# Optimization experiments

Measured on AMD Instinct MI355X. Metric: run time of the kernel, lower is better.

The kernel has to match this reference:

```python
import jax, jax.numpy as jnp
import numpy as np

N = 50000      # nodes
E = 800000     # edges (before self loops)
B = 64         # graphs in batch
D_IN, D_HID, D_LAT, N_CLS = 3, 128, 64, 2


def _gat_params(key, d_in, d_out, scale=0.1):
    k1, k2, k3 = jax.random.split(key, 3)
    return (jax.random.normal(k1, (d_in, d_out), jnp.float32) * scale,
            jax.random.normal(k2, (d_out,), jnp.float32) * scale,
            jax.random.normal(k3, (d_out,), jnp.float32) * scale,
            jnp.zeros((d_out,), jnp.float32))


def setup_inputs() -> dict:
    key = jax.random.key(0)
    ks = jax.random.split(key, 10)
    x = jax.random.normal(ks[0], (N, D_IN), jnp.float32)
    edge_index = jax.random.randint(ks[1], (2, E), 0, N, dtype=jnp.int64)
    batch = jnp.sort(jax.random.randint(ks[2], (N,), 0, B, dtype=jnp.int64))
    W1, a1s, a1d, b1 = _gat_params(ks[3], D_IN, D_HID)
    W2, a2s, a2d, b2 = _gat_params(ks[4], D_HID, D_LAT)
    W3, a3s, a3d, b3 = _gat_params(ks[5], D_LAT, D_HID)
    W4, a4s, a4d, b4 = _gat_params(ks[6], D_HID, D_IN)
    kc1, kc2 = jax.random.split(ks[7])
    Wc1 = jax.random.normal(kc1, (D_LAT, D_LAT // 2), jnp.float32) * 0.1
    bc1 = jnp.zeros((D_LAT // 2,), jnp.float32)
    Wc2 = jax.random.normal(kc2, (D_LAT // 2, N_CLS), jnp.float32) * 0.1
    bc2 = jnp.zeros((N_CLS,), jnp.float32)
    return dict(x=x, edge_index=edge_index, batch=batch,
                W1=W1, a1s=a1s, a1d=a1d, b1=b1,
                W2=W2, a2s=a2s, a2d=a2d, b2=b2,
                W3=W3, a3s=a3s, a3d=a3d, b3=b3,
                W4=W4, a4s=a4s, a4d=a4d, b4=b4,
                Wc1=Wc1, bc1=bc1, Wc2=Wc2, bc2=bc2)


def gat_conv(x, W, a_src, a_dst, bias, send, recv, n):
    # Single-head PyG GATConv: h = xW; e_ij = LeakyReLU(a_src.h_j + a_dst.h_i);
    # alpha = softmax over incoming edges of i; out_i = sum_j alpha_ij h_j + b
    h = x @ W                                   # [n, d_out]
    e = jax.nn.leaky_relu(jnp.take(h @ a_src, send) + jnp.take(h @ a_dst, recv), 0.2)
    m = jax.ops.segment_max(e, recv, num_segments=n)   # stable softmax per dst
    e = jnp.exp(e - m[recv])
    s = jax.ops.segment_sum(e, recv, num_segments=n)
    alpha = e / s[recv]                         # [E+N]
    out = jax.ops.segment_sum(alpha[:, None] * h[send], recv, num_segments=n)
    return out + bias


def reference(x, edge_index, batch,
              W1, a1s, a1d, b1, W2, a2s, a2d, b2,
              W3, a3s, a3d, b3, W4, a4s, a4d, b4,
              Wc1, bc1, Wc2, bc2):
    loop = jnp.arange(N, dtype=edge_index.dtype)
    send = jnp.concatenate([edge_index[0], loop])   # add_self_loops=True
    recv = jnp.concatenate([edge_index[1], loop])
    # encode (dropout inactive in eval)
    h = jax.nn.relu(gat_conv(x, W1, a1s, a1d, b1, send, recv, N))
    latent = gat_conv(h, W2, a2s, a2d, b2, send, recv, N)
    # decode
    h = jax.nn.relu(gat_conv(latent, W3, a3s, a3d, b3, send, recv, N))
    reconstructed = gat_conv(h, W4, a4s, a4d, b4, send, recv, N)
    # per-graph mean pooling (segment mean, replaces Python loop)
    cnt = jax.ops.segment_sum(jnp.ones((N,), latent.dtype), batch, num_segments=B)
    pooled = jax.ops.segment_sum(latent, batch, num_segments=B) / jnp.maximum(cnt, 1.0)[:, None]
    z = jax.nn.relu(pooled @ Wc1 + bc1)
    noise_pred = z @ Wc2 + bc2
    return reconstructed, latent, noise_pred
```

## Files before the change

### kernel.cpp

```cpp
#include <hip/hip_runtime.h>
#include <hip/hip_bf16.h>

typedef __hip_bfloat16 bf16;

#define N_NODES 50000
#define N_EDGES 800000
#define NB 64

#define NBUCK 256
#define BUCK_R ((N_NODES + NBUCK - 1) / NBUCK)
#define BUCK_CAP 4352
#define OVF_CAP 65536
#define NBLK1 256
#define CHUNK1 ((N_EDGES + NBLK1 - 1) / NBLK1)
#define NIT ((CHUNK1 + 255) / 256)

#define XN_BLKS ((N_NODES + 255) / 256)
#define PREP_BLKS (XN_BLKS + 20 + 1)

#define P_W1 0
#define P_A1S 384
#define P_A1D 512
#define P_B1 640
#define P_W2 768
#define P_A2S 8960
#define P_A2D 9024
#define P_B2 9088
#define P_W3 9152
#define P_A3S 17344
#define P_A3D 17472
#define P_B3 17600
#define P_W4 17728
#define P_A4S 18112
#define P_A4D 18115
#define P_B4 18118
#define P_WC1 18121
#define P_BC1 20169
#define P_WC2 20201
#define P_BC2 20265
#define P_W1S 20272
#define P_W1D 20276
#define P_W3S 20280
#define P_W3D 20344
#define P_TOTAL 20408

__device__ __forceinline__ float wave_sum(float v) {
#pragma unroll
    for (int o = 32; o >= 1; o >>= 1) v += __shfl_xor(v, o, 64);
    return v;
}

__device__ __forceinline__ unsigned int pk2(float a, float b) {
    bf16 x = __float2bfloat16(a);
    bf16 y = __float2bfloat16(b);
    unsigned short ux = *reinterpret_cast<unsigned short*>(&x);
    unsigned short uy = *reinterpret_cast<unsigned short*>(&y);
    return ((unsigned int)uy << 16) | ux;
}
__device__ __forceinline__ float bf_lo(unsigned int u) {
    unsigned int v = u << 16;
    return *reinterpret_cast<float*>(&v);
}
__device__ __forceinline__ float bf_hi(unsigned int u) {
    unsigned int v = u & 0xffff0000u;
    return *reinterpret_cast<float*>(&v);
}

__device__ __forceinline__ int ld_idx(const void* p, long long i, int is64) {
    return is64 ? (int)((const long long*)p)[i] : ((const int*)p)[i];
}
__device__ __forceinline__ float ldf(const void* p, int i, int isbf) {
    return isbf ? __bfloat162float(((const bf16*)p)[i]) : ((const float*)p)[i];
}
__device__ __forceinline__ void st_out(void* p, long long i, float v, int isbf) {
    if (isbf) ((bf16*)p)[i] = __float2bfloat16(v);
    else ((float*)p)[i] = v;
}

__device__ __forceinline__ float attn_p(float esv, float edi) {
    float v = esv + edi;
    float e = (v >= 0.f) ? v : 0.2f * v;
    return __expf(fminf(e, 60.f));
}

struct PTab {
    const void* src[20];
    int off[20];
    int n[20];
};

__global__ __launch_bounds__(256) void k_prep(
        const void* __restrict__ x, const void* __restrict__ eidx,
        const void* __restrict__ rW1, const void* __restrict__ rA1s,
        const void* __restrict__ rA1d, const void* __restrict__ rW3,
        const void* __restrict__ rA3s, const void* __restrict__ rA3d,
        PTab tab, float* __restrict__ pblock, float* __restrict__ x4,
        int* __restrict__ gcur, int* __restrict__ ovf_cnt, int* __restrict__ flags) {
    __shared__ int scnt[2];
    const int t = threadIdx.x;
    if (t < 2) scnt[t] = 0;
    __syncthreads();
    {
        const unsigned short* xr = (const unsigned short*)x;
        unsigned int hb = (xr[2 * t] >> 8) & 0x7F;
        if (hb >= 58 && hb <= 65) atomicAdd(&scnt[0], 1);
        if (t < 64) {
            const unsigned int* er = (const unsigned int*)eidx;
            if (er[2 * t + 1] == 0u) atomicAdd(&scnt[1], 1);
        }
    }
    __syncthreads();
    const int isbf = (scnt[0] >= 200) ? 1 : 0;
    const int is64 = (scnt[1] >= 60) ? 1 : 0;

    const int b = blockIdx.x;
    if (b < XN_BLKS) {
        int node = b * 256 + t;
        if (node < N_NODES) {
            float4 v;
            v.x = ldf(x, node * 3 + 0, isbf);
            v.y = ldf(x, node * 3 + 1, isbf);
            v.z = ldf(x, node * 3 + 2, isbf);
            v.w = 0.f;
            *(float4*)&x4[node * 4] = v;
        }
    } else if (b < XN_BLKS + 20) {
        int p = b - XN_BLKS;
        const void* s = tab.src[p];
        float* d = pblock + tab.off[p];
        int n = tab.n[p];
        for (int i = t; i < n; i += 256) d[i] = ldf(s, i, isbf);
    } else {
        if (t < NBUCK) gcur[t] = 0;
        if (t == 0) { *ovf_cnt = 0; flags[0] = isbf; flags[1] = is64; }
        if (t < 3) {
            float s = 0.f, d = 0.f;
            for (int k = 0; k < 128; k++) {
                float wv = ldf(rW1, t * 128 + k, isbf);
                s = fmaf(wv, ldf(rA1s, k, isbf), s);
                d = fmaf(wv, ldf(rA1d, k, isbf), d);
            }
            pblock[P_W1S + t] = s;
            pblock[P_W1D + t] = d;
        }
        if (t >= 64 && t < 128) {
            int k = t - 64;
            float s = 0.f, d = 0.f;
            for (int c = 0; c < 128; c++) {
                float wv = ldf(rW3, k * 128 + c, isbf);
                s = fmaf(wv, ldf(rA3s, c, isbf), s);
                d = fmaf(wv, ldf(rA3d, c, isbf), d);
            }
            pblock[P_W3S + k] = s;
            pblock[P_W3D + k] = d;
        }
    }
}

__global__ __launch_bounds__(256) void k_bucket(
        const void* __restrict__ eidx, const int* __restrict__ flags,
        int* __restrict__ gcur, unsigned int* __restrict__ stage,
        int* __restrict__ ovf_cnt, uint2* __restrict__ ovf) {
    __shared__ int hist[NBUCK];
    __shared__ int base[NBUCK];
    const int t = threadIdx.x;
    const int is64 = flags[1];
    const int e0 = blockIdx.x * CHUNK1;
    const int e1 = min(e0 + CHUNK1, N_EDGES);

    unsigned int ent[NIT];
    int bk[NIT];
    hist[t] = 0;
    __syncthreads();
#pragma unroll
    for (int it = 0; it < NIT; it++) {
        int e = e0 + t + it * 256;
        int b = -1;
        unsigned int en = 0;
        if (e < e1) {
            int r = ld_idx(eidx, (long long)N_EDGES + e, is64);
            int s = ld_idx(eidx, e, is64);
            b = r / BUCK_R;
            en = ((unsigned)(r - b * BUCK_R) << 16) | (unsigned)s;
            atomicAdd(&hist[b], 1);
        }
        ent[it] = en;
        bk[it] = b;
    }
    __syncthreads();
    int cnt = hist[t];
    base[t] = (cnt > 0) ? atomicAdd(&gcur[t], cnt) : 0;
    __syncthreads();
    hist[t] = 0;
    __syncthreads();
#pragma unroll
    for (int it = 0; it < NIT; it++) {
        int b = bk[it];
        if (b >= 0) {
            int l = atomicAdd(&hist[b], 1);
            int slot = base[b] + l;
            if (slot < BUCK_CAP) {
                stage[(size_t)b * BUCK_CAP + slot] = ent[it];
            } else {
                int oi = atomicAdd(ovf_cnt, 1);
                int r = b * BUCK_R + (int)(ent[it] >> 16);
                if (oi < OVF_CAP) ovf[oi] = make_uint2(ent[it] & 0xffffu, (unsigned)r);
            }
        }
    }
}

__global__ __launch_bounds__(256) void k_count2(
        const int* __restrict__ gcur, const unsigned int* __restrict__ stage,
        const int* __restrict__ ovf_cnt, const uint2* __restrict__ ovf,
        int* __restrict__ loff, int* __restrict__ bsum) {
    __shared__ int hist[256];
    __shared__ int ss[256];
    const int b = blockIdx.x;
    const int r0 = b * BUCK_R;
    const int nr = min(BUCK_R, N_NODES - r0);
    const int t = threadIdx.x;
    hist[t] = 0;
    __syncthreads();
    const int cnt = min(gcur[b], BUCK_CAP);
    const unsigned int* sb = stage + (size_t)b * BUCK_CAP;
    for (int i = t; i < cnt; i += 256) atomicAdd(&hist[sb[i] >> 16], 1);
    int oc = min(*ovf_cnt, OVF_CAP);
    for (int i = t; i < oc; i += 256) {
        int r = (int)ovf[i].y;
        if (r >= r0 && r < r0 + nr) atomicAdd(&hist[r - r0], 1);
    }
    __syncthreads();
    int v = (t < nr) ? hist[t] + 1 : 0;
    ss[t] = v;
    __syncthreads();
#pragma unroll
    for (int o = 1; o < 256; o <<= 1) {
        int add = (t >= o) ? ss[t - o] : 0;
        __syncthreads();
        ss[t] += add;
        __syncthreads();
    }
    if (t < nr) loff[r0 + t] = ss[t] - v;
    if (t == 255) bsum[b] = ss[255];
}

__global__ __launch_bounds__(256) void k_fill3(
        const int* __restrict__ gcur, const unsigned int* __restrict__ stage,
        const int* __restrict__ ovf_cnt, const uint2* __restrict__ ovf,
        const int* __restrict__ loff, const int* __restrict__ bsum,
        int* __restrict__ off, int* __restrict__ csr_send) {
    __shared__ int sbs[NBUCK];
    __shared__ int ss[NBUCK];
    __shared__ int sstart[BUCK_R];
    __shared__ int lcur[BUCK_R];
    const int b = blockIdx.x;
    const int t = threadIdx.x;
    int v = bsum[t];
    sbs[t] = v;
    ss[t] = v;
    __syncthreads();
#pragma unroll
    for (int o = 1; o < NBUCK; o <<= 1) {
        int add = (t >= o) ? ss[t - o] : 0;
        __syncthreads();
        ss[t] += add;
        __syncthreads();
    }
    const int bb = ss[b] - sbs[b];
    if (b == NBUCK - 1 && t == 0) off[N_NODES] = ss[NBUCK - 1];

    const int r0 = b * BUCK_R;
    const int nr = min(BUCK_R, N_NODES - r0);
    for (int i = t; i < nr; i += 256) {
        int st = bb + loff[r0 + i];
        sstart[i] = st;
        off[r0 + i] = st;
        lcur[i] = 1;
        csr_send[st] = r0 + i;
    }
    __syncthreads();
    const int cnt = min(gcur[b], BUCK_CAP);
    const unsigned int* sb = stage + (size_t)b * BUCK_CAP;
    for (int i = t; i < cnt; i += 256) {
        unsigned int e = sb[i];
        int rl = (int)(e >> 16);
        int l = atomicAdd(&lcur[rl], 1);
        csr_send[sstart[rl] + l] = (int)(e & 0xffffu);
    }
    int oc = min(*ovf_cnt, OVF_CAP);
    for (int i = t; i < oc; i += 256) {
        uint2 pr = ovf[i];
        int r = (int)pr.y;
        if (r >= r0 && r < r0 + nr) {
            int rl = r - r0;
            int l = atomicAdd(&lcur[rl], 1);
            csr_send[sstart[rl] + l] = (int)pr.x;
        }
    }
}

__global__ __launch_bounds__(256) void k_esed1(
        const float* __restrict__ x4, const float* __restrict__ pb,
        float* __restrict__ es, float* __restrict__ ed) {
    int node = blockIdx.x * 256 + threadIdx.x;
    if (node >= N_NODES) return;
    float4 v = *(const float4*)&x4[node * 4];
    es[node] = v.x * pb[P_W1S] + v.y * pb[P_W1S + 1] + v.z * pb[P_W1S + 2];
    ed[node] = v.x * pb[P_W1D] + v.y * pb[P_W1D + 1] + v.z * pb[P_W1D + 2];
}

__global__ __launch_bounds__(256) void k_esed3(
        const float* __restrict__ latent, const float* __restrict__ pb,
        float* __restrict__ es, float* __restrict__ ed) {
    int wid = threadIdx.x >> 6, lane = threadIdx.x & 63;
    int node = blockIdx.x * 4 + wid;
    if (node >= N_NODES) return;
    float lv = latent[(size_t)node * 64 + lane];
    float s = lv * pb[P_W3S + lane];
    float d = lv * pb[P_W3D + lane];
    s = wave_sum(s);
    d = wave_sum(d);
    if (lane == 0) { es[node] = s; ed[node] = d; }
}

__global__ __launch_bounds__(256) void k_wsumx3(
        const float* __restrict__ x4, const float* __restrict__ es,
        const float* __restrict__ ed, const int* __restrict__ off,
        const int* __restrict__ csr_send, float* __restrict__ xagg) {
    int wid = threadIdx.x >> 6, lane = threadIdx.x & 63;
    int node = blockIdx.x * 4 + wid;
    if (node >= N_NODES) return;
    int start = off[node], end = off[node + 1];
    float edi = ed[node];
    float a0 = 0.f, a1 = 0.f, a2 = 0.f, sl = 0.f;
    for (int j = start + lane; j < end; j += 64) {
        int s = csr_send[j];
        float p = attn_p(es[s], edi);
        sl += p;
        float4 xv = *(const float4*)&x4[s * 4];
        a0 = fmaf(p, xv.x, a0);
        a1 = fmaf(p, xv.y, a1);
        a2 = fmaf(p, xv.z, a2);
    }
    float S = wave_sum(sl);
    a0 = wave_sum(a0);
    a1 = wave_sum(a1);
    a2 = wave_sum(a2);
    if (lane == 0) {
        float inv = 1.f / S;
        float4 r = {a0 * inv, a1 * inv, a2 * inv, 0.f};
        *(float4*)&xagg[node * 4] = r;
    }
}

template <int DIN, int DINS, int DOUT, int MODE>
__global__ __launch_bounds__(256) void k_gemm(
        const float* __restrict__ in, const float* __restrict__ W,
        const float* __restrict__ as_, const float* __restrict__ ad_,
        const float* __restrict__ bias, void* __restrict__ hout,
        float* __restrict__ es, float* __restrict__ ed) {
    constexpr int KC = (DIN < 32) ? DIN : 32;
    constexpr int NCH = DIN / KC;
    constexpr int CG = (DOUT >= 64) ? (DOUT / 8) : 1;
    constexpr int NT = (DOUT >= 64) ? ((256 / CG) * 4) : 256;
    constexpr int NTP = NT + 4;

    __shared__ float sX[KC][NTP];
    __shared__ float sW[KC][DOUT];

    const int t = threadIdx.x;
    const int node0 = blockIdx.x * NT;
    const int nvalid = min(NT, N_NODES - node0);

    const int cg = t & (CG - 1);
    const int ng = t / CG;

    float acc[4][8] = {};

    for (int ch = 0; ch < NCH; ch++) {
        const int k0 = ch * KC;
        if (ch > 0) __syncthreads();
        for (int i = t; i < nvalid * KC; i += 256) {
            int n = i / KC, k = i - n * KC;
            sX[k][n] = in[(size_t)(node0 + n) * DINS + k0 + k];
        }
        for (int i = t; i < KC * DOUT; i += 256) {
            int k = i / DOUT, c = i - k * DOUT;
            sW[k][c] = W[(size_t)(k0 + k) * DOUT + c];
        }
        __syncthreads();

        if constexpr (DOUT >= 64) {
#pragma unroll 4
            for (int k = 0; k < KC; k++) {
                float4 xv = *(const float4*)&sX[k][ng * 4];
                float4 w0 = *(const float4*)&sW[k][cg * 8];
                float4 w1 = *(const float4*)&sW[k][cg * 8 + 4];
                float xs[4] = {xv.x, xv.y, xv.z, xv.w};
                float ws[8] = {w0.x, w0.y, w0.z, w0.w, w1.x, w1.y, w1.z, w1.w};
#pragma unroll
                for (int j = 0; j < 4; j++)
#pragma unroll
                    for (int c = 0; c < 8; c++)
                        acc[j][c] = fmaf(xs[j], ws[c], acc[j][c]);
            }
        } else {
#pragma unroll 4
            for (int k = 0; k < KC; k++) {
                float xv = sX[k][t];
#pragma unroll
                for (int c = 0; c < DOUT; c++)
                    acc[0][c] = fmaf(xv, sW[k][c], acc[0][c]);
            }
        }
    }

    if constexpr (DOUT >= 64) {
        if constexpr (MODE == 2) {
            float bv[8];
#pragma unroll
            for (int c = 0; c < 8; c++) bv[c] = bias[cg * 8 + c];
            float* out = (float*)hout;
#pragma unroll
            for (int j = 0; j < 4; j++) {
                int n = ng * 4 + j;
                if (n < nvalid) {
                    float4 v0, v1;
                    v0.x = fmaxf(acc[j][0] + bv[0], 0.f);
                    v0.y = fmaxf(acc[j][1] + bv[1], 0.f);
                    v0.z = fmaxf(acc[j][2] + bv[2], 0.f);
                    v0.w = fmaxf(acc[j][3] + bv[3], 0.f);
                    v1.x = fmaxf(acc[j][4] + bv[4], 0.f);
                    v1.y = fmaxf(acc[j][5] + bv[5], 0.f);
                    v1.z = fmaxf(acc[j][6] + bv[6], 0.f);
                    v1.w = fmaxf(acc[j][7] + bv[7], 0.f);
                    *(float4*)&out[(size_t)(node0 + n) * DOUT + cg * 8] = v0;
                    *(float4*)&out[(size_t)(node0 + n) * DOUT + cg * 8 + 4] = v1;
                }
            }
        } else {
            float asv[8], adv[8];
#pragma unroll
            for (int c = 0; c < 8; c++) {
                asv[c] = as_[cg * 8 + c];
                adv[c] = ad_[cg * 8 + c];
            }
#pragma unroll
            for (int j = 0; j < 4; j++) {
                int n = ng * 4 + j;
                float e_s = 0.f, e_d = 0.f;
#pragma unroll
                for (int c = 0; c < 8; c++) {
                    e_s = fmaf(acc[j][c], asv[c], e_s);
                    e_d = fmaf(acc[j][c], adv[c], e_d);
                }
#pragma unroll
                for (int m = 1; m < CG; m <<= 1) {
                    e_s += __shfl_xor(e_s, m, 64);
                    e_d += __shfl_xor(e_d, m, 64);
                }
                if (n < nvalid) {
                    if (cg == 0) {
                        es[node0 + n] = e_s;
                        ed[node0 + n] = e_d;
                    }
                    unsigned short* hb = (unsigned short*)hout;
                    uint4 u;
                    u.x = pk2(acc[j][0], acc[j][1]);
                    u.y = pk2(acc[j][2], acc[j][3]);
                    u.z = pk2(acc[j][4], acc[j][5]);
                    u.w = pk2(acc[j][6], acc[j][7]);
                    *(uint4*)&hb[(size_t)(node0 + n) * DOUT + cg * 8] = u;
                }
            }
        }
    } else {
        if (t < nvalid) {
            int node = node0 + t;
            float e_s = 0.f, e_d = 0.f;
#pragma unroll
            for (int c = 0; c < DOUT; c++) {
                e_s = fmaf(acc[0][c], as_[c], e_s);
                e_d = fmaf(acc[0][c], ad_[c], e_d);
            }
            es[node] = e_s;
            ed[node] = e_d;
            float* h = (float*)hout;
            float4 v = {acc[0][0], acc[0][1], acc[0][2], 0.f};
            *(float4*)&h[(size_t)node * 4] = v;
        }
    }
}

__global__ __launch_bounds__(256) void k_wsum64f(
        const unsigned short* __restrict__ hb, const float* __restrict__ es,
        const float* __restrict__ ed, const float* __restrict__ bias,
        const int* __restrict__ off, const int* __restrict__ csr_send,
        float* __restrict__ out, unsigned short* __restrict__ lat16,
        void* __restrict__ out_dev, long long out_off, const int* __restrict__ flags) {
    int wid = threadIdx.x >> 6, lane = threadIdx.x & 63;
    int node = blockIdx.x * 4 + wid;
    if (node >= N_NODES) return;
    int start = off[node], end = off[node + 1];
    float edi = ed[node];

    const int qd = lane >> 4;
    const int ql = lane & 15;
    float4 a0 = {0.f, 0.f, 0.f, 0.f}, a1 = {0.f, 0.f, 0.f, 0.f};
    float4 a2 = {0.f, 0.f, 0.f, 0.f}, a3 = {0.f, 0.f, 0.f, 0.f};
    float sl = 0.f;

    for (int base = start; base < end; base += 64) {
        int j = base + lane;
        bool valid = j < end;
        int src = valid ? csr_send[j] : 0;
        float p = valid ? attn_p(es[src], edi) : 0.f;
        sl += p;
        int cnt = min(64, end - base);
        int nq = (cnt + 3) >> 2;
        int j2 = 0;
        for (; j2 + 4 <= nq; j2 += 4) {
            int qA = 4 * j2 + qd;
            float pA = __shfl(p, qA, 64);      int sA = __shfl(src, qA, 64);
            float pB = __shfl(p, qA + 4, 64);  int sB = __shfl(src, qA + 4, 64);
            float pC = __shfl(p, qA + 8, 64);  int sC = __shfl(src, qA + 8, 64);
            float pD = __shfl(p, qA + 12, 64); int sD = __shfl(src, qA + 12, 64);
            uint2 uA = *((const uint2*)(hb + (size_t)sA * 64) + ql);
            uint2 uB = *((const uint2*)(hb + (size_t)sB * 64) + ql);
            uint2 uC = *((const uint2*)(hb + (size_t)sC * 64) + ql);
            uint2 uD = *((const uint2*)(hb + (size_t)sD * 64) + ql);
            a0.x = fmaf(pA, bf_lo(uA.x), a0.x); a0.y = fmaf(pA, bf_hi(uA.x), a0.y);
            a0.z = fmaf(pA, bf_lo(uA.y), a0.z); a0.w = fmaf(pA, bf_hi(uA.y), a0.w);
            a1.x = fmaf(pB, bf_lo(uB.x), a1.x); a1.y = fmaf(pB, bf_hi(uB.x), a1.y);
            a1.z = fmaf(pB, bf_lo(uB.y), a1.z); a1.w = fmaf(pB, bf_hi(uB.y), a1.w);
            a2.x = fmaf(pC, bf_lo(uC.x), a2.x); a2.y = fmaf(pC, bf_hi(uC.x), a2.y);
            a2.z = fmaf(pC, bf_lo(uC.y), a2.z); a2.w = fmaf(pC, bf_hi(uC.y), a2.w);
            a3.x = fmaf(pD, bf_lo(uD.x), a3.x); a3.y = fmaf(pD, bf_hi(uD.x), a3.y);
            a3.z = fmaf(pD, bf_lo(uD.y), a3.z); a3.w = fmaf(pD, bf_hi(uD.y), a3.w);
        }
        for (; j2 < nq; j2++) {
            int q = 4 * j2 + qd;
            float pq = __shfl(p, q, 64); int sq = __shfl(src, q, 64);
            uint2 u = *((const uint2*)(hb + (size_t)sq * 64) + ql);
            a0.x = fmaf(pq, bf_lo(u.x), a0.x); a0.y = fmaf(pq, bf_hi(u.x), a0.y);
            a0.z = fmaf(pq, bf_lo(u.y), a0.z); a0.w = fmaf(pq, bf_hi(u.y), a0.w);
        }
    }
    float S = wave_sum(sl);
    float inv = 1.f / S;
    float4 r;
    r.x = (a0.x + a1.x) + (a2.x + a3.x);
    r.y = (a0.y + a1.y) + (a2.y + a3.y);
    r.z = (a0.z + a1.z) + (a2.z + a3.z);
    r.w = (a0.w + a1.w) + (a2.w + a3.w);
    r.x += __shfl_xor(r.x, 16, 64); r.y += __shfl_xor(r.y, 16, 64);
    r.z += __shfl_xor(r.z, 16, 64); r.w += __shfl_xor(r.w, 16, 64);
    r.x += __shfl_xor(r.x, 32, 64); r.y += __shfl_xor(r.y, 32, 64);
    r.z += __shfl_xor(r.z, 32, 64); r.w += __shfl_xor(r.w, 32, 64);
    if (qd == 0) {
        float4 b = ((const float4*)bias)[ql];
        r.x = fmaf(r.x, inv, b.x); r.y = fmaf(r.y, inv, b.y);
        r.z = fmaf(r.z, inv, b.z); r.w = fmaf(r.w, inv, b.w);
        ((float4*)(out + (size_t)node * 64))[ql] = r;
        uint2 u = {pk2(r.x, r.y), pk2(r.z, r.w)};
        ((uint2*)(lat16 + (size_t)node * 64))[ql] = u;
        int isbf = flags[0];
        long long o4 = out_off + (long long)node * 64 + 4 * ql;
        st_out(out_dev, o4 + 0, r.x, isbf);
        st_out(out_dev, o4 + 1, r.y, isbf);
        st_out(out_dev, o4 + 2, r.z, isbf);
        st_out(out_dev, o4 + 3, r.w, isbf);
    }
}

__global__ __launch_bounds__(256) void k_wsumx64(
        const unsigned short* __restrict__ lat16, const float* __restrict__ es,
        const float* __restrict__ ed, const int* __restrict__ off,
        const int* __restrict__ csr_send, float* __restrict__ lagg) {
    int wid = threadIdx.x >> 6, lane = threadIdx.x & 63;
    int node = blockIdx.x * 4 + wid;
    if (node >= N_NODES) return;
    int start = off[node], end = off[node + 1];
    float edi = ed[node];

    const int qd = lane >> 4;
    const int ql = lane & 15;
    float4 a0 = {0.f, 0.f, 0.f, 0.f}, a1 = {0.f, 0.f, 0.f, 0.f};
    float4 a2 = {0.f, 0.f, 0.f, 0.f}, a3 = {0.f, 0.f, 0.f, 0.f};
    float sl = 0.f;

    for (int base = start; base < end; base += 64) {
        int j = base + lane;
        bool valid = j < end;
        int src = valid ? csr_send[j] : 0;
        float p = valid ? attn_p(es[src], edi) : 0.f;
        sl += p;
        int cnt = min(64, end - base);
        int nq = (cnt + 3) >> 2;
        int j2 = 0;
        for (; j2 + 4 <= nq; j2 += 4) {
            int qA = 4 * j2 + qd;
            float pA = __shfl(p, qA, 64);      int sA = __shfl(src, qA, 64);
            float pB = __shfl(p, qA + 4, 64);  int sB = __shfl(src, qA + 4, 64);
            float pC = __shfl(p, qA + 8, 64);  int sC = __shfl(src, qA + 8, 64);
            float pD = __shfl(p, qA + 12, 64); int sD = __shfl(src, qA + 12, 64);
            uint2 uA = *((const uint2*)(lat16 + (size_t)sA * 64) + ql);
            uint2 uB = *((const uint2*)(lat16 + (size_t)sB * 64) + ql);
            uint2 uC = *((const uint2*)(lat16 + (size_t)sC * 64) + ql);
            uint2 uD = *((const uint2*)(lat16 + (size_t)sD * 64) + ql);
            a0.x = fmaf(pA, bf_lo(uA.x), a0.x); a0.y = fmaf(pA, bf_hi(uA.x), a0.y);
            a0.z = fmaf(pA, bf_lo(uA.y), a0.z); a0.w = fmaf(pA, bf_hi(uA.y), a0.w);
            a1.x = fmaf(pB, bf_lo(uB.x), a1.x); a1.y = fmaf(pB, bf_hi(uB.x), a1.y);
            a1.z = fmaf(pB, bf_lo(uB.y), a1.z); a1.w = fmaf(pB, bf_hi(uB.y), a1.w);
            a2.x = fmaf(pC, bf_lo(uC.x), a2.x); a2.y = fmaf(pC, bf_hi(uC.x), a2.y);
            a2.z = fmaf(pC, bf_lo(uC.y), a2.z); a2.w = fmaf(pC, bf_hi(uC.y), a2.w);
            a3.x = fmaf(pD, bf_lo(uD.x), a3.x); a3.y = fmaf(pD, bf_hi(uD.x), a3.y);
            a3.z = fmaf(pD, bf_lo(uD.y), a3.z); a3.w = fmaf(pD, bf_hi(uD.y), a3.w);
        }
        for (; j2 < nq; j2++) {
            int q = 4 * j2 + qd;
            float pq = __shfl(p, q, 64); int sq = __shfl(src, q, 64);
            uint2 u = *((const uint2*)(lat16 + (size_t)sq * 64) + ql);
            a0.x = fmaf(pq, bf_lo(u.x), a0.x); a0.y = fmaf(pq, bf_hi(u.x), a0.y);
            a0.z = fmaf(pq, bf_lo(u.y), a0.z); a0.w = fmaf(pq, bf_hi(u.y), a0.w);
        }
    }
    float S = wave_sum(sl);
    float inv = 1.f / S;
    float4 r;
    r.x = (a0.x + a1.x) + (a2.x + a3.x);
    r.y = (a0.y + a1.y) + (a2.y + a3.y);
    r.z = (a0.z + a1.z) + (a2.z + a3.z);
    r.w = (a0.w + a1.w) + (a2.w + a3.w);
    r.x += __shfl_xor(r.x, 16, 64); r.y += __shfl_xor(r.y, 16, 64);
    r.z += __shfl_xor(r.z, 16, 64); r.w += __shfl_xor(r.w, 16, 64);
    r.x += __shfl_xor(r.x, 32, 64); r.y += __shfl_xor(r.y, 32, 64);
    r.z += __shfl_xor(r.z, 32, 64); r.w += __shfl_xor(r.w, 32, 64);
    if (qd == 0) {
        r.x *= inv; r.y *= inv; r.z *= inv; r.w *= inv;
        ((float4*)(lagg + (size_t)node * 64))[ql] = r;
    }
}

__global__ __launch_bounds__(256) void k_wsum3f(
        const float* __restrict__ h, const float* __restrict__ es,
        const float* __restrict__ ed, const float* __restrict__ bias,
        const int* __restrict__ off, const int* __restrict__ csr_send,
        void* __restrict__ out_dev, long long out_off, const int* __restrict__ flags) {
    int wid = threadIdx.x >> 6, lane = threadIdx.x & 63;
    int node = blockIdx.x * 4 + wid;
    if (node >= N_NODES) return;
    int start = off[node], end = off[node + 1];
    float edi = ed[node];

    float a0 = 0.f, a1 = 0.f, a2 = 0.f, sl = 0.f;
    for (int j = start + lane; j < end; j += 64) {
        int s = csr_send[j];
        float p = attn_p(es[s], edi);
        sl += p;
        float4 rv = *(const float4*)(h + (size_t)s * 4);
        a0 = fmaf(p, rv.x, a0);
        a1 = fmaf(p, rv.y, a1);
        a2 = fmaf(p, rv.z, a2);
    }
    float S = wave_sum(sl);
    a0 = wave_sum(a0);
    a1 = wave_sum(a1);
    a2 = wave_sum(a2);
    if (lane < 3) {
        float inv = 1.f / S;
        float v = fmaf((lane == 0 ? a0 : (lane == 1 ? a1 : a2)), inv, bias[lane]);
        st_out(out_dev, out_off + (long long)node * 3 + lane, v, flags[0]);
    }
}

#define POOL_W 16
__global__ void k_poolcls(const float* __restrict__ latent, const void* __restrict__ batch,
                          const int* __restrict__ flags, const float* __restrict__ pb,
                          void* __restrict__ out_dev, long long out_off) {
    int b = blockIdx.x;
    int lane = threadIdx.x & 63;
    int wave = threadIdx.x >> 6;
    int is64 = flags[1];
    int lo = 0, hi = N_NODES;
    while (lo < hi) { int mid = (lo + hi) >> 1; if (ld_idx(batch, mid, is64) < b) lo = mid + 1; else hi = mid; }
    int start = lo;
    lo = 0; hi = N_NODES;
    while (lo < hi) { int mid = (lo + hi) >> 1; if (ld_idx(batch, mid, is64) < b + 1) lo = mid + 1; else hi = mid; }
    int end = lo;
    float s = 0.f;
    for (int n = start + wave; n < end; n += POOL_W) s += latent[(size_t)n * 64 + lane];
    __shared__ float red[POOL_W][64];
    __shared__ float ps[64];
    red[wave][lane] = s;
    __syncthreads();
    if (wave == 0) {
        float t = s;
#pragma unroll
        for (int w2 = 1; w2 < POOL_W; w2++) t += red[w2][lane];
        float cnt = (float)(end - start);
        ps[lane] = t / fmaxf(cnt, 1.f);
    }
    __syncthreads();
    if (wave == 0 && lane < 32) {
        float z = pb[P_BC1 + lane];
        for (int c = 0; c < 64; c++) z = fmaf(ps[c], pb[P_WC1 + c * 32 + lane], z);
        z = fmaxf(z, 0.f);
        float p0 = z * pb[P_WC2 + lane * 2];
        float p1 = z * pb[P_WC2 + lane * 2 + 1];
#pragma unroll
        for (int o = 16; o >= 1; o >>= 1) {
            p0 += __shfl_xor(p0, o, 64);
            p1 += __shfl_xor(p1, o, 64);
        }
        if (lane == 0) {
            int isbf = flags[0];
            st_out(out_dev, out_off + b * 2 + 0, p0 + pb[P_BC2], isbf);
            st_out(out_dev, out_off + b * 2 + 1, p1 + pb[P_BC2 + 1], isbf);
        }
    }
}

extern "C" void kernel_launch(void* const* d_in, const int* in_sizes, int n_in,
                              void* d_out, int out_size, void* d_ws, size_t ws_size,
                              hipStream_t stream) {
    const void* x    = d_in[0];
    const void* eidx = d_in[1];
    const void* batch= d_in[2];

    char* w = (char*)d_ws;
    size_t o = 0;
    auto carve = [&](size_t bytes) { void* p = w + o; o = (o + bytes + 255) & ~(size_t)255; return p; };
    int* flags    = (int*)carve(8 * sizeof(int));
    int* off      = (int*)carve((N_NODES + 1) * sizeof(int));
    int* loff     = (int*)carve(N_NODES * sizeof(int));
    int* bsum     = (int*)carve(NBUCK * sizeof(int));
    int* gcur     = (int*)carve(NBUCK * sizeof(int));
    int* ovf_cnt  = (int*)carve(sizeof(int));
    int* csr_send = (int*)carve((size_t)(N_EDGES + N_NODES) * sizeof(int));
    unsigned int* stage = (unsigned int*)carve((size_t)NBUCK * BUCK_CAP * sizeof(unsigned int));
    uint2* ovf    = (uint2*)carve((size_t)OVF_CAP * sizeof(uint2));
    float* pblock = (float*)carve(P_TOTAL * sizeof(float));
    float* x4     = (float*)carve((size_t)N_NODES * 4 * sizeof(float));
    float* xagg   = (float*)carve((size_t)N_NODES * 4 * sizeof(float));
    float* buf0   = (float*)carve((size_t)N_NODES * 128 * sizeof(float));
    unsigned short* hb = (unsigned short*)carve((size_t)N_NODES * 64 * sizeof(unsigned short));
    unsigned short* lat16 = (unsigned short*)carve((size_t)N_NODES * 64 * sizeof(unsigned short));
    float* lagg   = (float*)carve((size_t)N_NODES * 64 * sizeof(float));
    float* h3     = (float*)carve((size_t)N_NODES * 4 * sizeof(float));
    float* es     = (float*)carve(N_NODES * sizeof(float));
    float* ed     = (float*)carve(N_NODES * sizeof(float));

    int gW = N_NODES / 4;

    PTab tab;
    const int pn[20]  = {384,128,128,128, 8192,64,64,64, 8192,128,128,128, 384,3,3,3, 2048,32,64,2};
    const int pof[20] = {P_W1,P_A1S,P_A1D,P_B1, P_W2,P_A2S,P_A2D,P_B2, P_W3,P_A3S,P_A3D,P_B3,
                         P_W4,P_A4S,P_A4D,P_B4, P_WC1,P_BC1,P_WC2,P_BC2};
    for (int i = 0; i < 20; i++) { tab.src[i] = d_in[3 + i]; tab.off[i] = pof[i]; tab.n[i] = pn[i]; }
    k_prep<<<PREP_BLKS, 256, 0, stream>>>(x, eidx, d_in[3], d_in[4], d_in[5],
                                          d_in[11], d_in[12], d_in[13],
                                          tab, pblock, x4, gcur, ovf_cnt, flags);

    k_bucket<<<NBLK1, 256, 0, stream>>>(eidx, flags, gcur, stage, ovf_cnt, ovf);
    k_count2<<<NBUCK, 256, 0, stream>>>(gcur, stage, ovf_cnt, ovf, loff, bsum);
    k_fill3<<<NBUCK, 256, 0, stream>>>(gcur, stage, ovf_cnt, ovf, loff, bsum, off, csr_send);

    const long long OFF_RECON = 0, OFF_LATENT = 150000, OFF_NOISE = 3350000;

    int g64  = (N_NODES + 63) / 64;
    int g128 = (N_NODES + 127) / 128;
    int g196 = (N_NODES + 255) / 256;
    int g256 = (N_NODES + 255) / 256;

    k_esed1<<<g196, 256, 0, stream>>>(x4, pblock, es, ed);
    k_wsumx3<<<gW, 256, 0, stream>>>(x4, es, ed, off, csr_send, xagg);
    k_gemm<3, 4, 128, 2><<<g64, 256, 0, stream>>>(xagg, pblock + P_W1, pblock, pblock,
                                                  pblock + P_B1, buf0, es, ed);

    k_gemm<128, 128, 64, 0><<<g128, 256, 0, stream>>>(buf0, pblock + P_W2, pblock + P_A2S,
                                                      pblock + P_A2D, pblock, hb, es, ed);
    k_wsum64f<<<gW, 256, 0, stream>>>(hb, es, ed, pblock + P_B2, off, csr_send,
                                      buf0, lat16, d_out, OFF_LATENT, flags);

    k_poolcls<<<NB, POOL_W * 64, 0, stream>>>(buf0, batch, flags, pblock, d_out, OFF_NOISE);

    k_esed3<<<gW, 256, 0, stream>>>(buf0, pblock, es, ed);
    k_wsumx64<<<gW, 256, 0, stream>>>(lat16, es, ed, off, csr_send, lagg);
    k_gemm<64, 64, 128, 2><<<g64, 256, 0, stream>>>(lagg, pblock + P_W3, pblock, pblock,
                                                    pblock + P_B3, buf0, es, ed);

    k_gemm<128, 128, 3, 1><<<g256, 256, 0, stream>>>(buf0, pblock + P_W4, pblock + P_A4S,
                                                     pblock + P_A4D, pblock, h3, es, ed);
    k_wsum3f<<<gW, 256, 0, stream>>>(h3, es, ed, pblock + P_B4, off, csr_send,
                                     d_out, OFF_RECON, flags);
}
```

Before: 251.3 us.

## Fuse attention-score kernels and layer-1 GEMM into neighbouring kernels

Layer-1 attention logits are now computed in k_prep, which folds W1·a into each block. The layer-1 dense transform (3→128, bias, ReLU) is applied inside the aggregation kernel, so the separate GEMM and its xagg buffer go away. Layer-3 logits are computed inside k_wsum64f from the finished latent rows, into new es2/ed2 buffers. This removes three launches and one intermediate round trip, but each prep block now recomputes the 6 dot products and the aggregation kernel writes 128 floats per node.

```diff
diff --git a/kernel.cpp b/kernel.cpp
--- a/kernel.cpp
+++ b/kernel.cpp
@@ -38,8 +38,6 @@
 #define P_BC1 20169
 #define P_WC2 20201
 #define P_BC2 20265
-#define P_W1S 20272
-#define P_W1D 20276
 #define P_W3S 20280
 #define P_W3D 20344
 #define P_TOTAL 20408
@@ -95,8 +93,10 @@
         const void* __restrict__ rA1d, const void* __restrict__ rW3,
         const void* __restrict__ rA3s, const void* __restrict__ rA3d,
         PTab tab, float* __restrict__ pblock, float* __restrict__ x4,
+        float* __restrict__ es, float* __restrict__ ed,
         int* __restrict__ gcur, int* __restrict__ ovf_cnt, int* __restrict__ flags) {
     __shared__ int scnt[2];
+    __shared__ float sw[6];
     const int t = threadIdx.x;
     if (t < 2) scnt[t] = 0;
     __syncthreads();
@@ -115,14 +115,24 @@
 
     const int b = blockIdx.x;
     if (b < XN_BLKS) {
+        if (t < 6) {
+            int row = (t < 3) ? t : t - 3;
+            const void* av = (t < 3) ? rA1s : rA1d;
+            float s = 0.f;
+            for (int k = 0; k < 128; k++)
+                s = fmaf(ldf(rW1, row * 128 + k, isbf), ldf(av, k, isbf), s);
+            sw[t] = s;
+        }
+        __syncthreads();
         int node = b * 256 + t;
         if (node < N_NODES) {
-            float4 v;
-            v.x = ldf(x, node * 3 + 0, isbf);
-            v.y = ldf(x, node * 3 + 1, isbf);
-            v.z = ldf(x, node * 3 + 2, isbf);
-            v.w = 0.f;
+            float x0 = ldf(x, node * 3 + 0, isbf);
+            float x1 = ldf(x, node * 3 + 1, isbf);
+            float x2 = ldf(x, node * 3 + 2, isbf);
+            float4 v = {x0, x1, x2, 0.f};
             *(float4*)&x4[node * 4] = v;
+            es[node] = x0 * sw[0] + x1 * sw[1] + x2 * sw[2];
+            ed[node] = x0 * sw[3] + x1 * sw[4] + x2 * sw[5];
         }
     } else if (b < XN_BLKS + 20) {
         int p = b - XN_BLKS;
@@ -133,16 +143,6 @@
     } else {
         if (t < NBUCK) gcur[t] = 0;
         if (t == 0) { *ovf_cnt = 0; flags[0] = isbf; flags[1] = is64; }
-        if (t < 3) {
-            float s = 0.f, d = 0.f;
-            for (int k = 0; k < 128; k++) {
-                float wv = ldf(rW1, t * 128 + k, isbf);
-                s = fmaf(wv, ldf(rA1s, k, isbf), s);
-                d = fmaf(wv, ldf(rA1d, k, isbf), d);
-            }
-            pblock[P_W1S + t] = s;
-            pblock[P_W1D + t] = d;
-        }
         if (t >= 64 && t < 128) {
             int k = t - 64;
             float s = 0.f, d = 0.f;
@@ -300,34 +300,11 @@
     }
 }
 
-__global__ __launch_bounds__(256) void k_esed1(
-        const float* __restrict__ x4, const float* __restrict__ pb,
-        float* __restrict__ es, float* __restrict__ ed) {
-    int node = blockIdx.x * 256 + threadIdx.x;
-    if (node >= N_NODES) return;
-    float4 v = *(const float4*)&x4[node * 4];
-    es[node] = v.x * pb[P_W1S] + v.y * pb[P_W1S + 1] + v.z * pb[P_W1S + 2];
-    ed[node] = v.x * pb[P_W1D] + v.y * pb[P_W1D + 1] + v.z * pb[P_W1D + 2];
-}
-
-__global__ __launch_bounds__(256) void k_esed3(
-        const float* __restrict__ latent, const float* __restrict__ pb,
-        float* __restrict__ es, float* __restrict__ ed) {
-    int wid = threadIdx.x >> 6, lane = threadIdx.x & 63;
-    int node = blockIdx.x * 4 + wid;
-    if (node >= N_NODES) return;
-    float lv = latent[(size_t)node * 64 + lane];
-    float s = lv * pb[P_W3S + lane];
-    float d = lv * pb[P_W3D + lane];
-    s = wave_sum(s);
-    d = wave_sum(d);
-    if (lane == 0) { es[node] = s; ed[node] = d; }
-}
-
 __global__ __launch_bounds__(256) void k_wsumx3(
         const float* __restrict__ x4, const float* __restrict__ es,
-        const float* __restrict__ ed, const int* __restrict__ off,
-        const int* __restrict__ csr_send, float* __restrict__ xagg) {
+        const float* __restrict__ ed, const float* __restrict__ pb,
+        const int* __restrict__ off, const int* __restrict__ csr_send,
+        float* __restrict__ out) {
     int wid = threadIdx.x >> 6, lane = threadIdx.x & 63;
     int node = blockIdx.x * 4 + wid;
     if (node >= N_NODES) return;
@@ -347,11 +324,15 @@
     a0 = wave_sum(a0);
     a1 = wave_sum(a1);
     a2 = wave_sum(a2);
-    if (lane == 0) {
-        float inv = 1.f / S;
-        float4 r = {a0 * inv, a1 * inv, a2 * inv, 0.f};
-        *(float4*)&xagg[node * 4] = r;
-    }
+    float inv = 1.f / S;
+    a0 *= inv; a1 *= inv; a2 *= inv;
+    const float* W1 = pb + P_W1;
+    const float* b1 = pb + P_B1;
+    int c0 = lane, c1 = lane + 64;
+    float v0 = fmaf(a0, W1[c0], fmaf(a1, W1[128 + c0], fmaf(a2, W1[256 + c0], b1[c0])));
+    float v1 = fmaf(a0, W1[c1], fmaf(a1, W1[128 + c1], fmaf(a2, W1[256 + c1], b1[c1])));
+    out[(size_t)node * 128 + c0] = fmaxf(v0, 0.f);
+    out[(size_t)node * 128 + c1] = fmaxf(v1, 0.f);
 }
 
 template <int DIN, int DINS, int DOUT, int MODE>
@@ -495,9 +476,10 @@
 
 __global__ __launch_bounds__(256) void k_wsum64f(
         const unsigned short* __restrict__ hb, const float* __restrict__ es,
-        const float* __restrict__ ed, const float* __restrict__ bias,
+        const float* __restrict__ ed, const float* __restrict__ pb,
         const int* __restrict__ off, const int* __restrict__ csr_send,
         float* __restrict__ out, unsigned short* __restrict__ lat16,
+        float* __restrict__ es2, float* __restrict__ ed2,
         void* __restrict__ out_dev, long long out_off, const int* __restrict__ flags) {
     int wid = threadIdx.x >> 6, lane = threadIdx.x & 63;
     int node = blockIdx.x * 4 + wid;
@@ -559,7 +541,7 @@
     r.x += __shfl_xor(r.x, 32, 64); r.y += __shfl_xor(r.y, 32, 64);
     r.z += __shfl_xor(r.z, 32, 64); r.w += __shfl_xor(r.w, 32, 64);
     if (qd == 0) {
-        float4 b = ((const float4*)bias)[ql];
+        float4 b = ((const float4*)(pb + P_B2))[ql];
         r.x = fmaf(r.x, inv, b.x); r.y = fmaf(r.y, inv, b.y);
         r.z = fmaf(r.z, inv, b.z); r.w = fmaf(r.w, inv, b.w);
         ((float4*)(out + (size_t)node * 64))[ql] = r;
@@ -571,6 +553,18 @@
         st_out(out_dev, o4 + 1, r.y, isbf);
         st_out(out_dev, o4 + 2, r.z, isbf);
         st_out(out_dev, o4 + 3, r.w, isbf);
+        const float* w3s = pb + P_W3S;
+        const float* w3d = pb + P_W3D;
+        float s3 = r.x * w3s[4 * ql] + r.y * w3s[4 * ql + 1] +
+                   r.z * w3s[4 * ql + 2] + r.w * w3s[4 * ql + 3];
+        float d3 = r.x * w3d[4 * ql] + r.y * w3d[4 * ql + 1] +
+                   r.z * w3d[4 * ql + 2] + r.w * w3d[4 * ql + 3];
+#pragma unroll
+        for (int o = 8; o >= 1; o >>= 1) {
+            s3 += __shfl_xor(s3, o, 64);
+            d3 += __shfl_xor(d3, o, 64);
+        }
+        if (ql == 0) { es2[node] = s3; ed2[node] = d3; }
     }
 }
 
@@ -743,7 +737,6 @@
     uint2* ovf    = (uint2*)carve((size_t)OVF_CAP * sizeof(uint2));
     float* pblock = (float*)carve(P_TOTAL * sizeof(float));
     float* x4     = (float*)carve((size_t)N_NODES * 4 * sizeof(float));
-    float* xagg   = (float*)carve((size_t)N_NODES * 4 * sizeof(float));
     float* buf0   = (float*)carve((size_t)N_NODES * 128 * sizeof(float));
     unsigned short* hb = (unsigned short*)carve((size_t)N_NODES * 64 * sizeof(unsigned short));
     unsigned short* lat16 = (unsigned short*)carve((size_t)N_NODES * 64 * sizeof(unsigned short));
@@ -751,6 +744,8 @@
     float* h3     = (float*)carve((size_t)N_NODES * 4 * sizeof(float));
     float* es     = (float*)carve(N_NODES * sizeof(float));
     float* ed     = (float*)carve(N_NODES * sizeof(float));
+    float* es2    = (float*)carve(N_NODES * sizeof(float));
+    float* ed2    = (float*)carve(N_NODES * sizeof(float));
 
     int gW = N_NODES / 4;
 
@@ -761,7 +756,7 @@
     for (int i = 0; i < 20; i++) { tab.src[i] = d_in[3 + i]; tab.off[i] = pof[i]; tab.n[i] = pn[i]; }
     k_prep<<<PREP_BLKS, 256, 0, stream>>>(x, eidx, d_in[3], d_in[4], d_in[5],
                                           d_in[11], d_in[12], d_in[13],
-                                          tab, pblock, x4, gcur, ovf_cnt, flags);
+                                          tab, pblock, x4, es, ed, gcur, ovf_cnt, flags);
 
     k_bucket<<<NBLK1, 256, 0, stream>>>(eidx, flags, gcur, stage, ovf_cnt, ovf);
     k_count2<<<NBUCK, 256, 0, stream>>>(gcur, stage, ovf_cnt, ovf, loff, bsum);
@@ -769,25 +764,20 @@
 
     const long long OFF_RECON = 0, OFF_LATENT = 150000, OFF_NOISE = 3350000;
 
+    int g128 = (N_NODES + 127) / 128;
     int g64  = (N_NODES + 63) / 64;
-    int g128 = (N_NODES + 127) / 128;
-    int g196 = (N_NODES + 255) / 256;
     int g256 = (N_NODES + 255) / 256;
 
-    k_esed1<<<g196, 256, 0, stream>>>(x4, pblock, es, ed);
-    k_wsumx3<<<gW, 256, 0, stream>>>(x4, es, ed, off, csr_send, xagg);
-    k_gemm<3, 4, 128, 2><<<g64, 256, 0, stream>>>(xagg, pblock + P_W1, pblock, pblock,
-                                                  pblock + P_B1, buf0, es, ed);
+    k_wsumx3<<<gW, 256, 0, stream>>>(x4, es, ed, pblock, off, csr_send, buf0);
 
     k_gemm<128, 128, 64, 0><<<g128, 256, 0, stream>>>(buf0, pblock + P_W2, pblock + P_A2S,
                                                       pblock + P_A2D, pblock, hb, es, ed);
-    k_wsum64f<<<gW, 256, 0, stream>>>(hb, es, ed, pblock + P_B2, off, csr_send,
-                                      buf0, lat16, d_out, OFF_LATENT, flags);
+    k_wsum64f<<<gW, 256, 0, stream>>>(hb, es, ed, pblock, off, csr_send,
+                                      buf0, lat16, es2, ed2, d_out, OFF_LATENT, flags);
 
     k_poolcls<<<NB, POOL_W * 64, 0, stream>>>(buf0, batch, flags, pblock, d_out, OFF_NOISE);
 
-    k_esed3<<<gW, 256, 0, stream>>>(buf0, pblock, es, ed);
-    k_wsumx64<<<gW, 256, 0, stream>>>(lat16, es, ed, off, csr_send, lagg);
+    k_wsumx64<<<gW, 256, 0, stream>>>(lat16, es2, ed2, off, csr_send, lagg);
     k_gemm<64, 64, 128, 2><<<g64, 256, 0, stream>>>(lagg, pblock + P_W3, pblock, pblock,
                                                     pblock + P_B3, buf0, es, ed);
 
```

Result: faster. 232.5 us (-7.5%).
